# Optimization experiments

Measured on AMD Instinct MI355X. Metric: run time of the kernel, lower is better.

Reference implementation:

```python
import jax, jax.numpy as jnp
import numpy as np
from jax import lax

N_QUBITS = 4
N_LAYERS = 1
K = 4       # kernel_size = n_qubits
S = 2       # stride
CDTYPE = jnp.complex64


def _rz(theta):
    # theta: (B,) or scalar -> (B,2,2) or (2,2) complex RZ matrix diag(e^{-i t/2}, e^{i t/2})
    p = jnp.exp(-0.5j * theta.astype(CDTYPE))
    q = jnp.exp(0.5j * theta.astype(CDTYPE))
    z = jnp.zeros_like(p)
    return jnp.stack([jnp.stack([p, z], -1), jnp.stack([z, q], -1)], -2)


def _ry(theta):
    c = jnp.cos(theta / 2).astype(CDTYPE)
    s = jnp.sin(theta / 2).astype(CDTYPE)
    return jnp.stack([jnp.stack([c, -s], -1), jnp.stack([s, c], -1)], -2)


def _apply_1q(state, U, wire):
    # state: (B,2,2,2,2); U: (B,2,2) per-sample or (2,2) shared
    s = jnp.moveaxis(state, 1 + wire, -1)
    if U.ndim == 3:
        s = jnp.einsum('bij,b...j->b...i', U, s)
    else:
        s = jnp.einsum('ij,b...j->b...i', U, s)
    return jnp.moveaxis(s, -1, 1 + wire)


def _apply_crz(state, theta, c, t):
    # CRZ is diagonal: diag(1,1,e^{-i t/2},e^{+i t/2}) in |control,target> basis
    one = jnp.ones((), CDTYPE)
    d = jnp.stack([jnp.stack([one, one]),
                   jnp.stack([jnp.exp(-0.5j * theta).astype(CDTYPE),
                              jnp.exp(0.5j * theta).astype(CDTYPE)])])  # (2,2)[ctrl,tgt]
    s = jnp.moveaxis(state, [1 + c, 1 + t], [-2, -1])
    return jnp.moveaxis(s * d, [-2, -1], [1 + c, 1 + t])


def _qcircuit(inputs, weights):
    # inputs: (B, 16) encoding angles; weights: (n_layers, 2*n_qubits)
    B, n_in = inputs.shape
    var_per_qubit = n_in // N_QUBITS + 1  # = 5 for 16 inputs
    # Hadamard on every qubit applied to |0000> gives the uniform state (amp = 1/4)
    state = jnp.full((B,) + (2,) * N_QUBITS, 0.25, dtype=CDTYPE)
    # data encoding: alternating RZ/RY per qubit
    for q in range(N_QUBITS):
        for i in range(var_per_qubit):
            idx = q * var_per_qubit + i
            if idx < n_in:
                theta = inputs[:, idx]
                U = _rz(theta) if i % 2 == 0 else _ry(theta)
                state = _apply_1q(state, U, q)
    # variational layer(s): ring of CRZ then RY on each wire
    for l in range(weights.shape[0]):
        for i in range(N_QUBITS):
            state = _apply_crz(state, weights[l, i], i, (i + 1) % N_QUBITS)
        for j in range(N_QUBITS):
            state = _apply_1q(state, _ry(weights[l, N_QUBITS + j]), j)
    # <Z_q> expectation values
    p = (state * jnp.conj(state)).real  # (B,2,2,2,2)
    evs = []
    for q in range(N_QUBITS):
        axes = tuple(a for a in range(1, 1 + N_QUBITS) if a != 1 + q)
        pq = jnp.sum(p, axis=axes)  # (B,2)
        evs.append(pq[:, 0] - pq[:, 1])
    return jnp.stack(evs, -1)  # (B, 4)


def reference(X, weights):
    # X: (B, 1, H, W)
    B = X.shape[0]
    # all sliding 4x4/stride-2 patches, feature order (c, kh, kw) matches torch.flatten
    patches = lax.conv_general_dilated_patches(X, (K, K), (S, S), 'VALID')  # (B,16,ox,oy)
    ox, oy = patches.shape[2], patches.shape[3]
    flat = jnp.transpose(patches, (0, 2, 3, 1)).reshape(B * ox * oy, -1)  # row-major patch order
    out = _qcircuit(flat, weights)  # (B*ox*oy, 4)
    # reproduce torch.cat(dim=1).view(bs, n_qubits, ox, oy) ordering exactly
    return out.reshape(B, ox * oy * N_QUBITS).reshape(B, N_QUBITS, ox, oy)


def setup_inputs() -> dict:
    key = jax.random.key(0)
    kx, kw = jax.random.split(key)
    X = jax.random.normal(kx, (128, 1, 192, 192), dtype=jnp.float32)
    weights = jax.random.normal(kw, (N_LAYERS, 2 * N_QUBITS), dtype=jnp.float32)
    return {"X": X, "weights": weights}
```

## Files before the change

kernel.cpp:

```cpp
#include <hip/hip_runtime.h>

namespace {

constexpr int IMG = 192;
constexpr int OX = 95;
constexpr int OY = 95;
constexpr int NPB = OX * OY;
constexpr int BATCH = 128;
constexpr int TOTAL = BATCH * NPB;
constexpr int NWG = (TOTAL + 255) / 256;

__device__ __forceinline__ float2 cmul(float2 a, float2 b) {
    return make_float2(a.x*b.x - a.y*b.y, a.x*b.y + a.y*b.x);
}

__global__ __launch_bounds__(256) void quanv_kernel(
    const float* __restrict__ X, const float* __restrict__ W,
    float* __restrict__ out)
{
    int orig = blockIdx.x;
    constexpr int Q8 = NWG / 8, R8 = NWG % 8;
    int xcd = orig & 7, lin = orig >> 3;
    int swz = (xcd < R8 ? xcd * (Q8 + 1) : R8 * (Q8 + 1) + (xcd - R8) * Q8) + lin;

    int tid = swz * 256 + threadIdx.x;
    if (tid >= TOTAL) return;
    int b  = tid / NPB;
    int p  = tid - b * NPB;
    int px = p / OY;
    int py = p - px * OY;

    const float* base = X + (size_t)b * (IMG*IMG) + (px*2) * IMG + py*2;

    float in[16];
#pragma unroll
    for (int di = 0; di < 4; ++di) {
        const float2* r = reinterpret_cast<const float2*>(base + di*IMG);
        float2 lo = r[0], hi = r[1];
        in[di*4+0] = lo.x; in[di*4+1] = lo.y;
        in[di*4+2] = hi.x; in[di*4+3] = hi.y;
    }

    float m[4];
    float2 cq[4];
#pragma unroll
    for (int q = 0; q < 3; ++q) {
        float s0,c0, s1,c1, s2,c2, s3,c3, s4,c4;
        __sincosf(       in[q*5+0], &s0, &c0);
        __sincosf(0.5f * in[q*5+1], &s1, &c1);
        __sincosf(       in[q*5+2], &s2, &c2);
        __sincosf(0.5f * in[q*5+3], &s3, &c3);
        __sincosf(       in[q*5+4], &s4, &c4);
        float2 u0 = make_float2(c1 - s1*c0, -s1*s0);
        float2 u1 = make_float2(s1 + c1*c0,  c1*s0);
        u1 = cmul(u1, make_float2(c2, s2));
        float2 n0 = make_float2(c3*u0.x - s3*u1.x, c3*u0.y - s3*u1.y);
        float2 n1 = make_float2(s3*u0.x + c3*u1.x, s3*u0.y + c3*u1.y);
        n1 = cmul(n1, make_float2(c4, s4));
        m[q]  = (n0.x*n0.x + n0.y*n0.y) - (n1.x*n1.x + n1.y*n1.y);
        cq[q] = make_float2(n0.x*n1.x + n0.y*n1.y, n0.x*n1.y - n0.y*n1.x);
    }
    {
        float sn, cs;
        __sincosf(in[15], &sn, &cs);
        m[3]  = 0.f;
        cq[3] = make_float2(cs, sn);
    }

    float cosw[4], sinw[4], Kq[4], S4[4];
    float2 Eh[4];
#pragma unroll
    for (int k = 0; k < 4; ++k) {
        float sh, ch, sry, cry;
        __sincosf(0.5f * W[k], &sh, &ch);
        __sincosf(W[4+k], &sry, &cry);
        cosw[k] = ch*ch - sh*sh;
        sinw[k] = 2.f * ch * sh;
        Eh[k]   = make_float2(ch, -sh);
        Kq[k]   = 0.5f  * cry;
        S4[k]   = 0.25f * sry;
    }

    float2 aC[4], aT[4];
#pragma unroll
    for (int j = 0; j < 4; ++j) {
        float hm = 0.5f * m[j];
        int jm = (j + 3) & 3;
        aC[j] = make_float2((1.f + cosw[j])  + hm * (1.f - cosw[j]),
                            sinw[j]  * (1.f - hm));
        aT[j] = make_float2((1.f + cosw[jm]) + hm * (1.f - cosw[jm]),
                            sinw[jm] * (1.f - hm));
    }

    float ev[4];
#pragma unroll
    for (int q = 0; q < 4; ++q) {
        float2 t = cmul(aC[(q+3)&3], aT[(q+1)&3]);
        t = cmul(t, Eh[q]);
        float cross = cq[q].x * t.x - cq[q].y * t.y;
        ev[q] = Kq[q] * m[q] - S4[q] * cross;
    }

    reinterpret_cast<float4*>(out)[tid] = make_float4(ev[0], ev[1], ev[2], ev[3]);
}

}

extern "C" void kernel_launch(void* const* d_in, const int* in_sizes, int n_in,
                              void* d_out, int out_size, void* d_ws, size_t ws_size,
                              hipStream_t stream) {
    const float* X = (const float*)d_in[0];
    const float* W = (const float*)d_in[1];
    float* out = (float*)d_out;
    quanv_kernel<<<NWG, 256, 0, stream>>>(X, W, out);
}
```

Measured before the change: 17.46 us.

## Tile patches per workgroup and precompute per-pixel half-angle sincos in LDS

Each workgroup now handles a 16x16 tile of output patches. It loads the shared 34x34 pixel halo once, computes sin/cos of each half angle per pixel and stores them in shared memory. Full-angle values are then rebuilt with double-angle identities, so each pixel's transcendental is computed once instead of once per overlapping patch. The weight trig moves to a single thread writing to shared memory. The costs are a barrier, some idle threads in edge tiles (96 outputs covered for 95), and an uncoalesced, strided output write pattern.

```diff
diff --git a/kernel.cpp b/kernel.cpp
--- a/kernel.cpp
+++ b/kernel.cpp
@@ -3,12 +3,16 @@
 namespace {
 
 constexpr int IMG = 192;
-constexpr int OX = 95;
-constexpr int OY = 95;
+constexpr int OX = 95, OY = 95;
 constexpr int NPB = OX * OY;
 constexpr int BATCH = 128;
-constexpr int TOTAL = BATCH * NPB;
-constexpr int NWG = (TOTAL + 255) / 256;
+constexpr int TPX = 16, TPY = 16;
+constexpr int NTX = 6, NTY = 6;
+constexpr int TILES = NTX * NTY;
+constexpr int NWG = BATCH * TILES;
+constexpr int PR = 2 * TPX + 2;
+constexpr int PC = 2 * TPY + 2;
+constexpr int NPIX = PR * PC;
 
 __device__ __forceinline__ float2 cmul(float2 a, float2 b) {
     return make_float2(a.x*b.x - a.y*b.y, a.x*b.y + a.y*b.x);
@@ -18,67 +22,90 @@
     const float* __restrict__ X, const float* __restrict__ W,
     float* __restrict__ out)
 {
+    __shared__ __align__(16) float2 pix[NPIX];
+    __shared__ float wc[24];
+
     int orig = blockIdx.x;
-    constexpr int Q8 = NWG / 8, R8 = NWG % 8;
-    int xcd = orig & 7, lin = orig >> 3;
-    int swz = (xcd < R8 ? xcd * (Q8 + 1) : R8 * (Q8 + 1) + (xcd - R8) * Q8) + lin;
+    int wg = (orig & 7) * (NWG / 8) + (orig >> 3);
 
-    int tid = swz * 256 + threadIdx.x;
-    if (tid >= TOTAL) return;
-    int b  = tid / NPB;
-    int p  = tid - b * NPB;
-    int px = p / OY;
-    int py = p - px * OY;
+    int b  = wg / TILES;
+    int t  = wg - b * TILES;
+    int tx = t / NTY;
+    int ty = t - tx * NTY;
+    const int r0 = 32 * tx, c0 = 32 * ty;
 
-    const float* base = X + (size_t)b * (IMG*IMG) + (px*2) * IMG + py*2;
+    if (threadIdx.x == 0) {
+#pragma unroll
+        for (int k = 0; k < 4; ++k) {
+            float sh, chh, sry, cry;
+            __sincosf(0.5f * W[k], &sh, &chh);
+            __sincosf(W[4 + k], &sry, &cry);
+            wc[k]      = chh*chh - sh*sh;
+            wc[4 + k]  = 2.f * chh * sh;
+            wc[8 + k]  = chh;
+            wc[12 + k] = -sh;
+            wc[16 + k] = 0.5f  * cry;
+            wc[20 + k] = 0.25f * sry;
+        }
+    }
 
-    float in[16];
+    const float* img = X + (size_t)b * (IMG * IMG);
+#pragma unroll
+    for (int e = threadIdx.x; e < NPIX; e += 256) {
+        int r = e / PC, c = e - r * PC;
+        int gr = min(r0 + r, IMG - 1);
+        int gc = min(c0 + c, IMG - 1);
+        float x = img[gr * IMG + gc];
+        float sh, chh;
+        __sincosf(0.5f * x, &sh, &chh);
+        pix[e] = make_float2(sh, chh);
+    }
+    __syncthreads();
+
+    int lpx = threadIdx.x >> 4, lpy = threadIdx.x & 15;
+    int px = tx * TPX + lpx, py = ty * TPY + lpy;
+    if (px >= OX || py >= OY) return;
+
+    float sh[16], ch[16];
+    const float4* p4 = reinterpret_cast<const float4*>(pix);
 #pragma unroll
     for (int di = 0; di < 4; ++di) {
-        const float2* r = reinterpret_cast<const float2*>(base + di*IMG);
-        float2 lo = r[0], hi = r[1];
-        in[di*4+0] = lo.x; in[di*4+1] = lo.y;
-        in[di*4+2] = hi.x; in[di*4+3] = hi.y;
+        int base2 = ((2*lpx + di) * PC + 2*lpy) >> 1;
+        float4 a = p4[base2], bb = p4[base2 + 1];
+        sh[di*4+0] = a.x;  ch[di*4+0] = a.y;
+        sh[di*4+1] = a.z;  ch[di*4+1] = a.w;
+        sh[di*4+2] = bb.x; ch[di*4+2] = bb.y;
+        sh[di*4+3] = bb.z; ch[di*4+3] = bb.w;
     }
 
     float m[4];
     float2 cq[4];
 #pragma unroll
     for (int q = 0; q < 3; ++q) {
-        float s0,c0, s1,c1, s2,c2, s3,c3, s4,c4;
-        __sincosf(       in[q*5+0], &s0, &c0);
-        __sincosf(0.5f * in[q*5+1], &s1, &c1);
-        __sincosf(       in[q*5+2], &s2, &c2);
-        __sincosf(0.5f * in[q*5+3], &s3, &c3);
-        __sincosf(       in[q*5+4], &s4, &c4);
-        float2 u0 = make_float2(c1 - s1*c0, -s1*s0);
-        float2 u1 = make_float2(s1 + c1*c0,  c1*s0);
-        u1 = cmul(u1, make_float2(c2, s2));
+        const int f = q * 5;
+        float c0f = ch[f]*ch[f] - sh[f]*sh[f];
+        float s0f = 2.f * sh[f] * ch[f];
+        float s1 = sh[f+1], c1 = ch[f+1];
+        float c2f = ch[f+2]*ch[f+2] - sh[f+2]*sh[f+2];
+        float s2f = 2.f * sh[f+2] * ch[f+2];
+        float s3 = sh[f+3], c3 = ch[f+3];
+        float c4f = ch[f+4]*ch[f+4] - sh[f+4]*sh[f+4];
+        float s4f = 2.f * sh[f+4] * ch[f+4];
+
+        float2 u0 = make_float2(c1 - s1*c0f, -s1*s0f);
+        float2 u1 = make_float2(s1 + c1*c0f,  c1*s0f);
+        u1 = cmul(u1, make_float2(c2f, s2f));
         float2 n0 = make_float2(c3*u0.x - s3*u1.x, c3*u0.y - s3*u1.y);
         float2 n1 = make_float2(s3*u0.x + c3*u1.x, s3*u0.y + c3*u1.y);
-        n1 = cmul(n1, make_float2(c4, s4));
+        n1 = cmul(n1, make_float2(c4f, s4f));
         m[q]  = (n0.x*n0.x + n0.y*n0.y) - (n1.x*n1.x + n1.y*n1.y);
         cq[q] = make_float2(n0.x*n1.x + n0.y*n1.y, n0.x*n1.y - n0.y*n1.x);
     }
     {
-        float sn, cs;
-        __sincosf(in[15], &sn, &cs);
+        float c = ch[15]*ch[15] - sh[15]*sh[15];
+        float s = 2.f * sh[15] * ch[15];
         m[3]  = 0.f;
-        cq[3] = make_float2(cs, sn);
-    }
-
-    float cosw[4], sinw[4], Kq[4], S4[4];
-    float2 Eh[4];
-#pragma unroll
-    for (int k = 0; k < 4; ++k) {
-        float sh, ch, sry, cry;
-        __sincosf(0.5f * W[k], &sh, &ch);
-        __sincosf(W[4+k], &sry, &cry);
-        cosw[k] = ch*ch - sh*sh;
-        sinw[k] = 2.f * ch * sh;
-        Eh[k]   = make_float2(ch, -sh);
-        Kq[k]   = 0.5f  * cry;
-        S4[k]   = 0.25f * sry;
+        cq[3] = make_float2(c, s);
     }
 
     float2 aC[4], aT[4];
@@ -86,22 +113,23 @@
     for (int j = 0; j < 4; ++j) {
         float hm = 0.5f * m[j];
         int jm = (j + 3) & 3;
-        aC[j] = make_float2((1.f + cosw[j])  + hm * (1.f - cosw[j]),
-                            sinw[j]  * (1.f - hm));
-        aT[j] = make_float2((1.f + cosw[jm]) + hm * (1.f - cosw[jm]),
-                            sinw[jm] * (1.f - hm));
+        float cwj = wc[j],  swj = wc[4 + j];
+        float cwm = wc[jm], swm = wc[4 + jm];
+        aC[j] = make_float2((1.f + cwj) + hm * (1.f - cwj), swj * (1.f - hm));
+        aT[j] = make_float2((1.f + cwm) + hm * (1.f - cwm), swm * (1.f - hm));
     }
 
     float ev[4];
 #pragma unroll
     for (int q = 0; q < 4; ++q) {
-        float2 t = cmul(aC[(q+3)&3], aT[(q+1)&3]);
-        t = cmul(t, Eh[q]);
-        float cross = cq[q].x * t.x - cq[q].y * t.y;
-        ev[q] = Kq[q] * m[q] - S4[q] * cross;
+        float2 tt = cmul(aC[(q+3)&3], aT[(q+1)&3]);
+        tt = cmul(tt, make_float2(wc[8+q], wc[12+q]));
+        float cross = cq[q].x * tt.x - cq[q].y * tt.y;
+        ev[q] = wc[16+q] * m[q] - wc[20+q] * cross;
     }
 
-    reinterpret_cast<float4*>(out)[tid] = make_float4(ev[0], ev[1], ev[2], ev[3]);
+    reinterpret_cast<float4*>(out)[b * NPB + px * OY + py] =
+        make_float4(ev[0], ev[1], ev[2], ev[3]);
 }
 
 }
```

Result: slower. 19.25 us (+10.3%).

## Compute two horizontally adjacent patches per thread sharing half-angle sincos

Applied to the files above, without the earlier changes.

Each thread now handles two neighbouring stride-2 patches in a row, loading a 4x6 window once and computing sincos of half-angles for all 24 values. Full angles are rebuilt with double-angle identities, so the overlapping columns are shared and the number of transcendental calls per patch roughly drops. The grid halves, the XCD swizzle is simplified to an exact chunk mapping, and the last column's second patch is masked. This trades more registers and fewer threads against less redundant sincos work and fewer loads.

```diff
diff --git a/kernel.cpp b/kernel.cpp
--- a/kernel.cpp
+++ b/kernel.cpp
@@ -3,15 +3,70 @@
 namespace {
 
 constexpr int IMG = 192;
-constexpr int OX = 95;
-constexpr int OY = 95;
+constexpr int OX = 95, OY = 95;
 constexpr int NPB = OX * OY;
 constexpr int BATCH = 128;
-constexpr int TOTAL = BATCH * NPB;
-constexpr int NWG = (TOTAL + 255) / 256;
+constexpr int JP = 48;
+constexpr int PERIMG = OX * JP;
+constexpr int TOTAL = BATCH * PERIMG;
+constexpr int NWG = TOTAL / 256;
+constexpr int CHUNK = NWG / 8;
 
 __device__ __forceinline__ float2 cmul(float2 a, float2 b) {
     return make_float2(a.x*b.x - a.y*b.y, a.x*b.y + a.y*b.x);
+}
+
+__device__ __forceinline__ void qubit_chain(
+    float s0, float c0, float s1, float c1, float s2, float c2,
+    float s3, float c3, float s4, float c4,
+    float& m, float2& cq)
+{
+    float C0 = c0*c0 - s0*s0, S0 = 2.f*s0*c0;
+    float C2 = c2*c2 - s2*s2, S2 = 2.f*s2*c2;
+    float C4 = c4*c4 - s4*s4, S4f = 2.f*s4*c4;
+    float2 u0 = make_float2(c1 - s1*C0, -s1*S0);
+    float2 u1 = make_float2(s1 + c1*C0,  c1*S0);
+    u1 = cmul(u1, make_float2(C2, S2));
+    float2 n0 = make_float2(c3*u0.x - s3*u1.x, c3*u0.y - s3*u1.y);
+    float2 n1 = make_float2(s3*u0.x + c3*u1.x, s3*u0.y + c3*u1.y);
+    n1 = cmul(n1, make_float2(C4, S4f));
+    m  = (n0.x*n0.x + n0.y*n0.y) - (n1.x*n1.x + n1.y*n1.y);
+    cq = make_float2(n0.x*n1.x + n0.y*n1.y, n0.x*n1.y - n0.y*n1.x);
+}
+
+__device__ __forceinline__ float4 patch_ev(
+    const float sh[4][6], const float ch[4][6], int o,
+    const float cw[4], const float sw[4], const float ehx[4], const float ehy[4],
+    const float Kq[4], const float S4v[4])
+{
+    float m[4]; float2 cq[4];
+    qubit_chain(sh[0][o+0],ch[0][o+0], sh[0][o+1],ch[0][o+1], sh[0][o+2],ch[0][o+2],
+                sh[0][o+3],ch[0][o+3], sh[1][o+0],ch[1][o+0], m[0], cq[0]);
+    qubit_chain(sh[1][o+1],ch[1][o+1], sh[1][o+2],ch[1][o+2], sh[1][o+3],ch[1][o+3],
+                sh[2][o+0],ch[2][o+0], sh[2][o+1],ch[2][o+1], m[1], cq[1]);
+    qubit_chain(sh[2][o+2],ch[2][o+2], sh[2][o+3],ch[2][o+3], sh[3][o+0],ch[3][o+0],
+                sh[3][o+1],ch[3][o+1], sh[3][o+2],ch[3][o+2], m[2], cq[2]);
+    {
+        float s = sh[3][o+3], c = ch[3][o+3];
+        m[3]  = 0.f;
+        cq[3] = make_float2(c*c - s*s, 2.f*s*c);
+    }
+
+    float ev[4];
+#pragma unroll
+    for (int q = 0; q < 4; ++q) {
+        int jm = (q + 3) & 3, jp = (q + 1) & 3;
+        float hmC = 0.5f * m[jm];
+        float2 aC = make_float2((1.f + cw[jm]) + hmC * (1.f - cw[jm]),
+                                sw[jm] * (1.f - hmC));
+        float hmT = 0.5f * m[jp];
+        float2 aT = make_float2((1.f + cw[q]) + hmT * (1.f - cw[q]),
+                                sw[q] * (1.f - hmT));
+        float2 t = cmul(aC, aT);
+        t = cmul(t, make_float2(ehx[q], ehy[q]));
+        ev[q] = Kq[q] * m[q] - S4v[q] * (cq[q].x * t.x - cq[q].y * t.y);
+    }
+    return make_float4(ev[0], ev[1], ev[2], ev[3]);
 }
 
 __global__ __launch_bounds__(256) void quanv_kernel(
@@ -19,89 +74,54 @@
     float* __restrict__ out)
 {
     int orig = blockIdx.x;
-    constexpr int Q8 = NWG / 8, R8 = NWG % 8;
-    int xcd = orig & 7, lin = orig >> 3;
-    int swz = (xcd < R8 ? xcd * (Q8 + 1) : R8 * (Q8 + 1) + (xcd - R8) * Q8) + lin;
+    int wg = (orig & 7) * CHUNK + (orig >> 3);
+    int tid = wg * 256 + threadIdx.x;
+    int b  = tid / PERIMG;
+    int r  = tid - b * PERIMG;
+    int px = r / JP;
+    int j  = r - px * JP;
+    const bool hasB = (j < JP - 1);
 
-    int tid = swz * 256 + threadIdx.x;
-    if (tid >= TOTAL) return;
-    int b  = tid / NPB;
-    int p  = tid - b * NPB;
-    int px = p / OY;
-    int py = p - px * OY;
+    const float* img = X + (size_t)b * (IMG*IMG) + (2*px) * IMG + 4*j;
+    const int c45 = hasB ? 4 : 0;
 
-    const float* base = X + (size_t)b * (IMG*IMG) + (px*2) * IMG + py*2;
-
-    float in[16];
+    float raw[4][6];
 #pragma unroll
     for (int di = 0; di < 4; ++di) {
-        const float2* r = reinterpret_cast<const float2*>(base + di*IMG);
-        float2 lo = r[0], hi = r[1];
-        in[di*4+0] = lo.x; in[di*4+1] = lo.y;
-        in[di*4+2] = hi.x; in[di*4+3] = hi.y;
+        const float* rp = img + di * IMG;
+        float4 v  = *reinterpret_cast<const float4*>(rp);
+        float2 w2 = *reinterpret_cast<const float2*>(rp + c45);
+        raw[di][0] = v.x; raw[di][1] = v.y; raw[di][2] = v.z; raw[di][3] = v.w;
+        raw[di][4] = w2.x; raw[di][5] = w2.y;
     }
 
-    float m[4];
-    float2 cq[4];
+    float cw[4], sw[4], ehx[4], ehy[4], Kq[4], S4v[4];
 #pragma unroll
-    for (int q = 0; q < 3; ++q) {
-        float s0,c0, s1,c1, s2,c2, s3,c3, s4,c4;
-        __sincosf(       in[q*5+0], &s0, &c0);
-        __sincosf(0.5f * in[q*5+1], &s1, &c1);
-        __sincosf(       in[q*5+2], &s2, &c2);
-        __sincosf(0.5f * in[q*5+3], &s3, &c3);
-        __sincosf(       in[q*5+4], &s4, &c4);
-        float2 u0 = make_float2(c1 - s1*c0, -s1*s0);
-        float2 u1 = make_float2(s1 + c1*c0,  c1*s0);
-        u1 = cmul(u1, make_float2(c2, s2));
-        float2 n0 = make_float2(c3*u0.x - s3*u1.x, c3*u0.y - s3*u1.y);
-        float2 n1 = make_float2(s3*u0.x + c3*u1.x, s3*u0.y + c3*u1.y);
-        n1 = cmul(n1, make_float2(c4, s4));
-        m[q]  = (n0.x*n0.x + n0.y*n0.y) - (n1.x*n1.x + n1.y*n1.y);
-        cq[q] = make_float2(n0.x*n1.x + n0.y*n1.y, n0.x*n1.y - n0.y*n1.x);
-    }
-    {
-        float sn, cs;
-        __sincosf(in[15], &sn, &cs);
-        m[3]  = 0.f;
-        cq[3] = make_float2(cs, sn);
+    for (int k = 0; k < 4; ++k) {
+        float shh, chh, sry, cry;
+        __sincosf(0.5f * W[k], &shh, &chh);
+        __sincosf(W[4 + k], &sry, &cry);
+        cw[k]  = chh*chh - shh*shh;
+        sw[k]  = 2.f * chh * shh;
+        ehx[k] = chh;
+        ehy[k] = -shh;
+        Kq[k]  = 0.5f  * cry;
+        S4v[k] = 0.25f * sry;
     }
 
-    float cosw[4], sinw[4], Kq[4], S4[4];
-    float2 Eh[4];
+    float sh[4][6], ch[4][6];
 #pragma unroll
-    for (int k = 0; k < 4; ++k) {
-        float sh, ch, sry, cry;
-        __sincosf(0.5f * W[k], &sh, &ch);
-        __sincosf(W[4+k], &sry, &cry);
-        cosw[k] = ch*ch - sh*sh;
-        sinw[k] = 2.f * ch * sh;
-        Eh[k]   = make_float2(ch, -sh);
-        Kq[k]   = 0.5f  * cry;
-        S4[k]   = 0.25f * sry;
-    }
+    for (int di = 0; di < 4; ++di)
+#pragma unroll
+        for (int cc = 0; cc < 6; ++cc)
+            __sincosf(0.5f * raw[di][cc], &sh[di][cc], &ch[di][cc]);
 
-    float2 aC[4], aT[4];
-#pragma unroll
-    for (int j = 0; j < 4; ++j) {
-        float hm = 0.5f * m[j];
-        int jm = (j + 3) & 3;
-        aC[j] = make_float2((1.f + cosw[j])  + hm * (1.f - cosw[j]),
-                            sinw[j]  * (1.f - hm));
-        aT[j] = make_float2((1.f + cosw[jm]) + hm * (1.f - cosw[jm]),
-                            sinw[jm] * (1.f - hm));
-    }
+    float4 evA = patch_ev(sh, ch, 0, cw, sw, ehx, ehy, Kq, S4v);
+    float4 evB = patch_ev(sh, ch, 2, cw, sw, ehx, ehy, Kq, S4v);
 
-    float ev[4];
-#pragma unroll
-    for (int q = 0; q < 4; ++q) {
-        float2 t = cmul(aC[(q+3)&3], aT[(q+1)&3]);
-        t = cmul(t, Eh[q]);
-        float cross = cq[q].x * t.x - cq[q].y * t.y;
-        ev[q] = Kq[q] * m[q] - S4[q] * cross;
-    }
-
-    reinterpret_cast<float4*>(out)[tid] = make_float4(ev[0], ev[1], ev[2], ev[3]);
+    float4* o4 = reinterpret_cast<float4*>(out) + (size_t)b * NPB + px * OY + 2*j;
+    o4[0] = evA;
+    if (hasB) o4[1] = evB;
 }
 
 }
```

After: 16.80 us. -3.7%, faster.
